# Optimization experiments

Measured on AMD Instinct MI355X. Metric: run time of the kernel, lower is better.

## Reference

```python
import jax, jax.numpy as jnp
import numpy as np

B, L, D, H, HD, K, MLP = 4, 2048, 1024, 16, 64, 24, 4096


def setup_inputs() -> dict:
    key = jax.random.key(0)
    ks = jax.random.split(key, 17)
    f32 = jnp.float32
    rn = lambda k, s, sc=1.0: jax.random.normal(k, s, dtype=f32) * sc
    return {
        'inputs': rn(ks[0], (B, L, D)),
        'eig_vals': jax.random.uniform(ks[1], (K,), dtype=f32),  # positive eigenvalues
        'eig_vecs': rn(ks[2], (L, K), 1.0 / np.sqrt(L)),
        'w_filters': rn(ks[3], (K, D), 1.0 / np.sqrt(K)),        # lecun_normal-ish
        'w_inputs': rn(ks[4], (D, D), 1.0 / np.sqrt(D)),
        'ln1_scale': jnp.ones((D,), f32),
        'ln1_bias': jnp.zeros((D,), f32),
        'wq': rn(ks[5], (D, H, HD), 1.0 / np.sqrt(D)),
        'wk': rn(ks[6], (D, H, HD), 1.0 / np.sqrt(D)),
        'wv': rn(ks[7], (D, H, HD), 1.0 / np.sqrt(D)),
        'wo': rn(ks[8], (H, HD, D), 1.0 / np.sqrt(D)),
        'ln2_scale': jnp.ones((D,), f32),
        'ln2_bias': jnp.zeros((D,), f32),
        'mlp_w1': rn(ks[9], (D, MLP), 1.0 / np.sqrt(D)),
        'mlp_b1': jnp.zeros((MLP,), f32),
        'mlp_w2': rn(ks[10], (MLP, D), 1.0 / np.sqrt(MLP)),
        'mlp_b2': jnp.zeros((D,), f32),
    }


def _layer_norm(x, scale, bias, eps=1e-6):
    m = jnp.mean(x, axis=-1, keepdims=True)
    v = jnp.var(x, axis=-1, keepdims=True)
    return (x - m) * jax.lax.rsqrt(v + eps) * scale + bias


def reference(inputs, eig_vals, eig_vecs, w_filters, w_inputs,
              ln1_scale, ln1_bias, wq, wk, wv, wo,
              ln2_scale, ln2_bias, mlp_w1, mlp_b1, mlp_w2, mlp_b2):
    seq = inputs.shape[1]
    # --- STU spectral long convolution ---
    rescaled = eig_vecs * eig_vals[None, :] ** 0.25            # [L,K]
    filters = jnp.einsum('lk,kd->ld', rescaled, w_filters)      # [L,D]
    xi = jnp.einsum('bli,id->bld', inputs, w_inputs)            # [B,L,D]
    # causal per-channel conv: out[b,l,d] = sum_t filters[t,d]*xi[b,l-t,d]
    # == full convolve truncated to first L; do it as one batched FFT conv.
    n = 2 * seq
    F = jnp.fft.rfft(filters, n=n, axis=0)                      # [n//2+1, D]
    X = jnp.fft.rfft(xi, n=n, axis=1)                           # [B, n//2+1, D]
    projection = jnp.fft.irfft(X * F[None], n=n, axis=1)[:, :seq, :]
    stu_outs = projection                                       # make_stu_residual=False

    # --- self attention (pre-LN) ---
    x = _layer_norm(stu_outs, ln1_scale, ln1_bias)
    hd = wq.shape[-1]
    q = jnp.einsum('bld,dhk->blhk', x, wq) / jnp.sqrt(jnp.asarray(hd, x.dtype))
    k = jnp.einsum('bld,dhk->blhk', x, wk)
    v = jnp.einsum('bld,dhk->blhk', x, wv)
    attn = jax.nn.softmax(jnp.einsum('bqhk,bshk->bhqs', q, k), axis=-1)
    a = jnp.einsum('bhqs,bshk->bqhk', attn, v)
    a = jnp.einsum('bqhk,hkd->bqd', a, wo)
    x = a + stu_outs

    # --- MLP block (pre-LN) ---
    y = _layer_norm(x, ln2_scale, ln2_bias)
    y = jax.nn.gelu(jnp.einsum('bld,df->blf', y, mlp_w1) + mlp_b1)
    y = jnp.einsum('blf,fd->bld', y, mlp_w2) + mlp_b2
    return x + y
```

## Files before the change

kernel.cpp:

```cpp
#include <hip/hip_runtime.h>
#include <math.h>

#define B_ 4
#define L_ 2048
#define D_ 1024
#define H_ 16
#define HD_ 64
#define K_ 24
#define MLP_ 4096

typedef unsigned short u16;
typedef short s16x8 __attribute__((ext_vector_type(8)));
typedef float fx4 __attribute__((ext_vector_type(4)));
typedef _Float16 h2 __attribute__((ext_vector_type(2)));

__device__ __forceinline__ u16 f2bf(float f) {
    unsigned u = __float_as_uint(f);
    unsigned r = (u + 0x7fff + ((u >> 16) & 1)) >> 16;
    return (u16)r;
}

__device__ __forceinline__ u16 f2h(float f) {
    _Float16 hv = (_Float16)f;
    return __builtin_bit_cast(u16, hv);
}

__device__ __forceinline__ float gelu_t(float x) {
    float u = 0.7978845608028654f * (x + 0.044715f * x * x * x);
    return x / (1.f + __expf(-2.f * u));
}

__device__ __forceinline__ void gload_lds16(const void* g, void* l) {
    __builtin_amdgcn_global_load_lds(
        (const __attribute__((address_space(1))) unsigned int*)g,
        (__attribute__((address_space(3))) unsigned int*)l, 16, 0, 0);
}

#define SBAR() do { __builtin_amdgcn_sched_barrier(0); \
                    __builtin_amdgcn_s_barrier(); \
                    __builtin_amdgcn_sched_barrier(0); } while (0)

__global__ __launch_bounds__(256) void filters_T(const float* __restrict__ eig_vals,
                                                 const float* __restrict__ eig_vecs,
                                                 const float* __restrict__ w_filters,
                                                 u16* __restrict__ outT) {
    int l0 = blockIdx.x * 64, d0 = blockIdx.y * 64;
    __shared__ float ev25[K_];
    __shared__ float rr[64][25];
    __shared__ float wfs[K_][64];
    int tid = threadIdx.x;
    if (tid < K_) ev25[tid] = powf(eig_vals[tid], 0.25f);
    __syncthreads();
    for (int i = tid; i < 64 * K_; i += 256)
        rr[i / K_][i % K_] = eig_vecs[l0 * K_ + i];
    for (int i = tid; i < K_ * 64; i += 256) {
        int k = i >> 6, dd = i & 63;
        wfs[k][dd] = ev25[k] * w_filters[k * D_ + d0 + dd];
    }
    __syncthreads();
    int lane = tid & 63, w = tid >> 6;
    float acc[16];
#pragma unroll
    for (int i = 0; i < 16; i++) acc[i] = 0.f;
#pragma unroll
    for (int k = 0; k < K_; k++) {
        float rv = rr[lane][k];
#pragma unroll
        for (int i = 0; i < 16; i++) acc[i] += rv * wfs[k][w * 16 + i];
    }
#pragma unroll
    for (int i = 0; i < 16; i++)
        outT[(size_t)(d0 + w * 16 + i) * L_ + l0 + (lane ^ 63)] = f2h(acc[i]);
}

__global__ __launch_bounds__(256) void transpose_h(const u16* __restrict__ in,
                                                   u16* __restrict__ outT) {
    __shared__ u16 t[64][68];
    int m0 = blockIdx.x * 64, d0 = blockIdx.y * 64;
    int tid = threadIdx.x;
    int r = tid >> 3, c8 = (tid & 7) * 8;
#pragma unroll
    for (int p = 0; p < 2; p++) {
        uint4 X = *(const uint4*)&in[(size_t)(m0 + r + p * 32) * D_ + d0 + c8];
        *(uint2*)&t[r + p * 32][c8] = make_uint2(X.x, X.y);
        *(uint2*)&t[r + p * 32][c8 + 4] = make_uint2(X.z, X.w);
    }
    __syncthreads();
    int dr = tid >> 3, mc = (tid & 7) * 8;
#pragma unroll
    for (int p = 0; p < 2; p++) {
        int d = dr + p * 32;
        unsigned h[8];
#pragma unroll
        for (int j = 0; j < 8; j++) h[j] = t[mc + j][d];
        uint4 o;
        o.x = h[0] | (h[1] << 16); o.y = h[2] | (h[3] << 16);
        o.z = h[4] | (h[5] << 16); o.w = h[6] | (h[7] << 16);
        *(uint4*)&outT[(size_t)(d0 + d) * (size_t)(B_ * L_) + m0 + mc] = o;
    }
}

__global__ __launch_bounds__(256) void cast_bf16(const float* __restrict__ in,
                                                 u16* __restrict__ out) {
    int i = blockIdx.x * 256 + threadIdx.x;
    float4 v = ((const float4*)in)[i];
    ushort4 o;
    o.x = f2bf(v.x); o.y = f2bf(v.y); o.z = f2bf(v.z); o.w = f2bf(v.w);
    ((ushort4*)out)[i] = o;
}

struct CastJobs {
    const float* src[8];
    u16* dst[8];
    int R[8], C[8];
    int off[8];
};

__global__ __launch_bounds__(256) void cast_T_all(CastJobs J) {
    __shared__ float t[32][33];
    int bid = blockIdx.x;
    int j = 0;
#pragma unroll
    for (int k = 1; k < 8; k++)
        if (bid >= J.off[k]) j = k;
    int local = bid - J.off[j];
    int R = J.R[j], C = J.C[j];
    int nbx = C >> 5;
    int lsh = __ffs(nbx) - 1;
    int bx = local & (nbx - 1), by = local >> lsh;
    const float* in = J.src[j];
    u16* out = J.dst[j];
    int c0 = bx * 32, r0 = by * 32;
    int tx = threadIdx.x & 31, ty = threadIdx.x >> 5;
#pragma unroll
    for (int p = 0; p < 4; p++)
        t[ty + p * 8][tx] = in[(size_t)(r0 + ty + p * 8) * C + c0 + tx];
    __syncthreads();
#pragma unroll
    for (int p = 0; p < 4; p++)
        out[(size_t)(c0 + ty + p * 8) * R + r0 + tx] = f2bf(t[tx][ty + p * 8]);
}

__global__ __launch_bounds__(512, 2) void gemm_bf16(
    const u16* __restrict__ A, const u16* __restrict__ Bt,
    float* __restrict__ C, u16* __restrict__ Cb,
    int M, int N, int K, float alpha,
    const float* __restrict__ bias, const float* __restrict__ resid, int act,
    int qcols, int f16out) {
    __shared__ __align__(16) u16 lds[3 * 24576];
    const int SLOT = 24576;
    const int BOFF = 8192;

    int tid = threadIdx.x;
    int wid = tid >> 6, lane = tid & 63;
    int quad = lane >> 4, l15 = lane & 15;
    int rb = wid >> 2, cb = wid & 3;

    int bxs = blockIdx.x, bys = blockIdx.y;
    if ((gridDim.y & 7) == 0) {
        int bid = blockIdx.x + gridDim.x * blockIdx.y;
        int xcd = bid & 7, idx = bid >> 3;
        bys = xcd + 8 * (idx / gridDim.x);
        bxs = idx % gridDim.x;
    }
    int bm = bys * 128, bn = bxs * 256;
    int nt = K >> 6;

    int qoffe = (quad * 8) ^ ((l15 & 4) ? 16 : 0);
    int aRd = (rb * 64 + l15) * 64 + qoffe;
    int bRd = BOFF + (cb * 64 + l15) * 64 + qoffe;

    int srow = wid * 8 + (lane >> 3);
    int scole = ((lane & 7) * 8) ^ ((lane & 32) ? 16 : 0);
    const u16* Ag = A + (size_t)(bm + srow) * K + scole;
    const u16* Bg = Bt + (size_t)(bn + srow) * K + scole;
    int ldst = wid * 512;

#define STAGE_A(s, t, c) gload_lds16(Ag + (size_t)(c) * 64 * K + (size_t)(t) * 64, \
                                     &lds[(s) * SLOT + (c) * 4096 + ldst])
#define STAGE_B(s, t, c) gload_lds16(Bg + (size_t)(c) * 64 * K + (size_t)(t) * 64, \
                                     &lds[(s) * SLOT + BOFF + (c) * 4096 + ldst])

    STAGE_A(0, 0, 0); STAGE_A(0, 0, 1);
    STAGE_B(0, 0, 0); STAGE_B(0, 0, 1); STAGE_B(0, 0, 2); STAGE_B(0, 0, 3);
    STAGE_A(1, 1, 0); STAGE_A(1, 1, 1);
    STAGE_B(1, 1, 0); STAGE_B(1, 1, 1); STAGE_B(1, 1, 2); STAGE_B(1, 1, 3);
    asm volatile("s_waitcnt vmcnt(6)" ::: "memory");
    SBAR();

    fx4 acc[4][4];
#pragma unroll
    for (int i = 0; i < 4; i++)
#pragma unroll
        for (int j = 0; j < 4; j++) acc[i][j] = (fx4){0.f, 0.f, 0.f, 0.f};

    int sa = 0, sb = 1, sc = 2;
    for (int t = 0; t < nt; t++) {
        int ts = (t + 2 < nt) ? t + 2 : nt - 1;
        const u16* ap = &lds[sa * SLOT + aRd];
        const u16* bp = &lds[sa * SLOT + bRd];
        s16x8 a[4], b[2][4];
#pragma unroll
        for (int mf = 0; mf < 4; mf++) a[mf] = *(const s16x8*)(ap + mf * 1024);
#pragma unroll
        for (int kk = 0; kk < 2; kk++)
#pragma unroll
            for (int nf = 0; nf < 4; nf++)
                b[kk][nf] = *(const s16x8*)(bp + nf * 1024 + kk * 32);
        STAGE_A(sc, ts, 0); STAGE_A(sc, ts, 1); STAGE_B(sc, ts, 0);
        SBAR();
        asm volatile("s_waitcnt lgkmcnt(0)" ::: "memory");
        __builtin_amdgcn_sched_barrier(0);
        __builtin_amdgcn_s_setprio(1);
#pragma unroll
        for (int nf = 0; nf < 4; nf++)
#pragma unroll
            for (int mf = 0; mf < 4; mf++)
                acc[mf][nf] = __builtin_amdgcn_mfma_f32_16x16x32_bf16(
                    a[mf], b[0][nf], acc[mf][nf], 0, 0, 0);
        __builtin_amdgcn_s_setprio(0);
        SBAR();
#pragma unroll
        for (int mf = 0; mf < 4; mf++)
            a[mf] = *(const s16x8*)(ap + mf * 1024 + 32);
        STAGE_B(sc, ts, 1); STAGE_B(sc, ts, 2); STAGE_B(sc, ts, 3);
        SBAR();
        asm volatile("s_waitcnt lgkmcnt(0)" ::: "memory");
        __builtin_amdgcn_sched_barrier(0);
        __builtin_amdgcn_s_setprio(1);
#pragma unroll
        for (int nf = 0; nf < 4; nf++)
#pragma unroll
            for (int mf = 0; mf < 4; mf++)
                acc[mf][nf] = __builtin_amdgcn_mfma_f32_16x16x32_bf16(
                    a[mf], b[1][nf], acc[mf][nf], 0, 0, 0);
        __builtin_amdgcn_s_setprio(0);
        asm volatile("s_waitcnt vmcnt(6)" ::: "memory");
        __builtin_amdgcn_sched_barrier(0);
        SBAR();
        int tmp = sa; sa = sb; sb = sc; sc = tmp;
    }
#undef STAGE_A
#undef STAGE_B

#pragma unroll
    for (int mf = 0; mf < 4; mf++) {
        int row0 = bm + rb * 64 + mf * 16 + quad * 4;
#pragma unroll
        for (int nf = 0; nf < 4; nf++) {
            int col = bn + cb * 64 + nf * 16 + l15;
            float a2 = (col < qcols) ? alpha * 0.125f : alpha;
            float bv = bias ? bias[col] : 0.f;
#pragma unroll
            for (int reg = 0; reg < 4; reg++) {
                float v = a2 * acc[mf][nf][reg] + bv;
                if (act) v = gelu_t(v);
                size_t idx = (size_t)(row0 + reg) * N + col;
                if (resid) v += resid[idx];
                if (C) C[idx] = v;
                else Cb[idx] = f16out ? f2h(v) : f2bf(v);
            }
        }
    }
}

__global__ __launch_bounds__(256, 6) void conv_k(const u16* __restrict__ FT,
                                                 const u16* __restrict__ XT,
                                                 float* __restrict__ OUT) {
    int bid = blockIdx.x + 16 * (blockIdx.y + 16 * blockIdx.z);
    int xcd = bid & 7, ix = bid >> 3;
    int group = xcd * 8 + (ix >> 4);
    int xblk = ix & 15;
    int d0 = (group & 15) * 64, b = group >> 4;

    __shared__ u16 xs[64][132];
    __shared__ u16 ftr[64][68];
    int tid = threadIdx.x;
    int dd = tid & 63;
    int jg = tid >> 6;
    int L0 = jg * 16;
    int frow = tid >> 3, fq = (tid & 7) * 8;
    int xrow = tid >> 4, xq = (tid & 15) * 8;
    const u16* fbase = FT + (size_t)(d0 + frow) * L_ + fq;
    const u16* xbase = XT + (size_t)(d0 + xrow) * (B_ * L_) + (size_t)b * L_ + xq;

#pragma unroll 1
    for (int half = 0; half < 2; half++) {
        int lt = half ? (31 - xblk) : xblk;
        int l0 = lt * 64;
        float acc[16];
#pragma unroll
        for (int i = 0; i < 16; i++) acc[i] = 0.f;

        for (int t0 = 0; t0 <= l0; t0 += 64) {
            int jb = l0 - t0 - 64;
#pragma unroll
            for (int p = 0; p < 2; p++) {
                uint4 Fq = *(const uint4*)(fbase + (size_t)p * 32 * L_ + t0);
                *(uint2*)&ftr[frow + p * 32][fq] = make_uint2(Fq.x, Fq.y);
                *(uint2*)&ftr[frow + p * 32][fq + 4] = make_uint2(Fq.z, Fq.w);
            }
            if (jb >= 0) {
#pragma unroll
                for (int p = 0; p < 4; p++) {
                    uint4 Xq = *(const uint4*)(xbase + (size_t)p * 16 * (B_ * L_) + jb);
                    *(uint2*)&xs[xrow + p * 16][xq] = make_uint2(Xq.x, Xq.y);
                    *(uint2*)&xs[xrow + p * 16][xq + 4] = make_uint2(Xq.z, Xq.w);
                }
            } else {
#pragma unroll
                for (int p = 0; p < 4; p++) {
                    uint4 Xq = make_uint4(0, 0, 0, 0);
                    if (xq >= 64)
                        Xq = *(const uint4*)(xbase + (size_t)p * 16 * (B_ * L_) - 64);
                    *(uint2*)&xs[xrow + p * 16][xq] = make_uint2(Xq.x, Xq.y);
                    *(uint2*)&xs[xrow + p * 16][xq + 4] = make_uint2(Xq.z, Xq.w);
                }
            }
            __syncthreads();

            unsigned Q[10], E[10];
            {
                uint2 q0 = *(const uint2*)&xs[dd][L0];
                uint2 q1 = *(const uint2*)&xs[dd][L0 + 4];
                uint2 q2 = *(const uint2*)&xs[dd][L0 + 8];
                uint2 q3 = *(const uint2*)&xs[dd][L0 + 12];
                Q[0] = q0.x; Q[1] = q0.y; Q[2] = q1.x; Q[3] = q1.y;
                Q[4] = q2.x; Q[5] = q2.y; Q[6] = q3.x; Q[7] = q3.y;
#pragma unroll
                for (int j = 0; j < 7; j++)
                    E[j] = __builtin_amdgcn_alignbit(Q[j + 1], Q[j], 16);
            }
#pragma unroll
            for (int s = 0; s < 16; s++) {
                const int h = (2 * s) % 10;
                uint2 nx = *(const uint2*)&xs[dd][L0 + 16 + 4 * s];
                Q[(h + 8) % 10] = nx.x;
                Q[(h + 9) % 10] = nx.y;
                E[(h + 7) % 10] = __builtin_amdgcn_alignbit(Q[(h + 8) % 10], Q[(h + 7) % 10], 16);
                E[(h + 8) % 10] = __builtin_amdgcn_alignbit(Q[(h + 9) % 10], Q[(h + 8) % 10], 16);
                uint2 fr = *(const uint2*)&ftr[dd][4 * s];
                h2 f01 = __builtin_bit_cast(h2, fr.x);
                h2 f23 = __builtin_bit_cast(h2, fr.y);
#pragma unroll
                for (int i = 0; i < 16; i += 2) {
                    const int p = (h + i / 2) % 10;
                    const int p1 = (h + i / 2 + 1) % 10;
                    const int p2 = (h + i / 2 + 2) % 10;
                    acc[i] = __builtin_amdgcn_fdot2(f01, __builtin_bit_cast(h2, E[p]), acc[i], false);
                    acc[i] = __builtin_amdgcn_fdot2(f23, __builtin_bit_cast(h2, E[p1]), acc[i], false);
                    acc[i + 1] = __builtin_amdgcn_fdot2(f01, __builtin_bit_cast(h2, Q[p1]), acc[i + 1], false);
                    acc[i + 1] = __builtin_amdgcn_fdot2(f23, __builtin_bit_cast(h2, Q[p2]), acc[i + 1], false);
                }
            }
            __syncthreads();
        }
#pragma unroll
        for (int i = 0; i < 16; i++)
            OUT[((size_t)b * L_ + l0 + L0 + i) * D_ + d0 + dd] = acc[i];
    }
}

__global__ __launch_bounds__(256) void layernorm_bf16(const float* __restrict__ x,
                                                      const float* __restrict__ scale,
                                                      const float* __restrict__ bias,
                                                      u16* __restrict__ y) {
    size_t row = blockIdx.x;
    int tid = threadIdx.x;
    const float4 v = *(const float4*)&x[row * D_ + tid * 4];
    float s = v.x + v.y + v.z + v.w;
    float q = v.x * v.x + v.y * v.y + v.z * v.z + v.w * v.w;
#pragma unroll
    for (int off = 32; off >= 1; off >>= 1) {
        s += __shfl_xor(s, off, 64);
        q += __shfl_xor(q, off, 64);
    }
    __shared__ float ss[4], sq[4];
    int w = tid >> 6;
    if ((tid & 63) == 0) { ss[w] = s; sq[w] = q; }
    __syncthreads();
    s = ss[0] + ss[1] + ss[2] + ss[3];
    q = sq[0] + sq[1] + sq[2] + sq[3];
    float mean = s * (1.f / D_);
    float var = q * (1.f / D_) - mean * mean;
    float r = rsqrtf(var + 1e-6f);
    const float4 sc = *(const float4*)&scale[tid * 4];
    const float4 bi = *(const float4*)&bias[tid * 4];
    ushort4 o;
    o.x = f2bf((v.x - mean) * r * sc.x + bi.x);
    o.y = f2bf((v.y - mean) * r * sc.y + bi.y);
    o.z = f2bf((v.z - mean) * r * sc.z + bi.z);
    o.w = f2bf((v.w - mean) * r * sc.w + bi.w);
    *(ushort4*)&y[row * D_ + tid * 4] = o;
}

__global__ __launch_bounds__(256) void attn_mfma(const u16* __restrict__ Qg,
                                                 const u16* __restrict__ Kg,
                                                 const u16* __restrict__ Vg,
                                                 u16* __restrict__ Og) {
    const int QSTR = 3072;
    int bxs = blockIdx.x, bys = blockIdx.y;
    {
        int bid = blockIdx.x + gridDim.x * blockIdx.y;
        int xcd = bid & 7, idx = bid >> 3;
        bys = xcd + 8 * (idx / gridDim.x);
        bxs = idx % gridDim.x;
    }
    int q0 = bxs * 128;
    int b = bys >> 4, h = bys & 15;
    __shared__ __align__(16) u16 qs[128 * 72];
    __shared__ __align__(16) u16 ks[64 * 72];
    __shared__ __align__(16) u16 vt[64 * 72];
    int tid = threadIdx.x;
    int w = tid >> 6, lane = tid & 63;
    int quad = lane >> 4, l15 = lane & 15;
    const size_t base = (size_t)b * L_ * QSTR + h * HD_;

#pragma unroll
    for (int i = tid; i < 128 * 8; i += 256) {
        int r = i >> 3, c = i & 7;
        *(uint4*)&qs[r * 72 + c * 8] =
            *(const uint4*)&Qg[base + (size_t)(q0 + r) * QSTR + c * 8];
    }
    __syncthreads();
    s16x8 aq[2][2];
#pragma unroll
    for (int mi = 0; mi < 2; mi++)
#pragma unroll
        for (int kb = 0; kb < 2; kb++)
            aq[mi][kb] = *(const s16x8*)&qs[(w * 32 + mi * 16 + l15) * 72 + kb * 32 + quad * 8];

    float rsacc[2][4];
    fx4 o[2][4];
#pragma unroll
    for (int mi = 0; mi < 2; mi++)
#pragma unroll
        for (int i = 0; i < 4; i++) {
            rsacc[mi][i] = 0.f;
            o[mi][i] = (fx4){0.f, 0.f, 0.f, 0.f};
        }
    u16* psw = qs + w * 32 * 72;

    int kr0 = tid >> 3, kc = tid & 7;
    const u16* kg0 = Kg + base + (size_t)kr0 * QSTR + kc * 8;
    const u16* kg1 = kg0 + (size_t)32 * QSTR;
    const u16* vg = Vg + base + (size_t)lane * QSTR + w * 8;
    uint4 kp0 = *(const uint4*)kg0;
    uint4 kp1 = *(const uint4*)kg1;
    uint4 vp0 = *(const uint4*)vg;
    uint4 vp1 = *(const uint4*)(vg + 32);

    for (int s0 = 0; s0 < L_; s0 += 64) {
        __syncthreads();
        *(uint4*)&ks[kr0 * 72 + kc * 8] = kp0;
        *(uint4*)&ks[(kr0 + 32) * 72 + kc * 8] = kp1;
        {
            u16 t0[8], t1[8];
            *(uint4*)t0 = vp0;
            *(uint4*)t1 = vp1;
#pragma unroll
            for (int j = 0; j < 8; j++) vt[(w * 8 + j) * 72 + lane] = t0[j];
#pragma unroll
            for (int j = 0; j < 8; j++) vt[(w * 8 + 32 + j) * 72 + lane] = t1[j];
        }
        if (s0 + 64 < L_) {
            size_t off = (size_t)(s0 + 64) * QSTR;
            kp0 = *(const uint4*)(kg0 + off);
            kp1 = *(const uint4*)(kg1 + off);
            vp0 = *(const uint4*)(vg + off);
            vp1 = *(const uint4*)(vg + off + 32);
        }
        __syncthreads();

        fx4 sv[2][4];
#pragma unroll
        for (int mi = 0; mi < 2; mi++)
#pragma unroll
            for (int nt = 0; nt < 4; nt++) sv[mi][nt] = (fx4){0.f, 0.f, 0.f, 0.f};
#pragma unroll
        for (int kb = 0; kb < 2; kb++)
#pragma unroll
            for (int nt = 0; nt < 4; nt++) {
                s16x8 bk = *(const s16x8*)&ks[(nt * 16 + l15) * 72 + kb * 32 + quad * 8];
#pragma unroll
                for (int mi = 0; mi < 2; mi++)
                    sv[mi][nt] = __builtin_amdgcn_mfma_f32_16x16x32_bf16(
                        aq[mi][kb], bk, sv[mi][nt], 0, 0, 0);
            }

#pragma unroll
        for (int mi = 0; mi < 2; mi++)
#pragma unroll
            for (int nt = 0; nt < 4; nt++)
#pragma unroll
                for (int reg = 0; reg < 4; reg++) {
                    float p = __expf(sv[mi][nt][reg]);
                    rsacc[mi][reg] += p;
                    psw[(mi * 16 + quad * 4 + reg) * 72 + nt * 16 + l15] = f2bf(p);
                }

#pragma unroll
        for (int kb = 0; kb < 2; kb++) {
            s16x8 ap[2];
#pragma unroll
            for (int mi = 0; mi < 2; mi++)
                ap[mi] = *(const s16x8*)&psw[(mi * 16 + l15) * 72 + kb * 32 + quad * 8];
#pragma unroll
            for (int nt = 0; nt < 4; nt++) {
                s16x8 bv = *(const s16x8*)&vt[(nt * 16 + l15) * 72 + kb * 32 + quad * 8];
#pragma unroll
                for (int mi = 0; mi < 2; mi++)
                    o[mi][nt] = __builtin_amdgcn_mfma_f32_16x16x32_bf16(
                        ap[mi], bv, o[mi][nt], 0, 0, 0);
            }
        }
    }
    float lsum[2][4];
#pragma unroll
    for (int mi = 0; mi < 2; mi++)
#pragma unroll
        for (int reg = 0; reg < 4; reg++) {
            float r = rsacc[mi][reg];
#pragma unroll
            for (int off = 8; off >= 1; off >>= 1)
                r += __shfl_xor(r, off, 16);
            lsum[mi][reg] = r;
        }
    const size_t baseo = (size_t)b * L_ * 1024 + h * HD_;
#pragma unroll
    for (int mi = 0; mi < 2; mi++)
#pragma unroll
        for (int reg = 0; reg < 4; reg++) {
            float inv = 1.f / lsum[mi][reg];
            size_t row = baseo +
                (size_t)(q0 + w * 32 + mi * 16 + quad * 4 + reg) * 1024;
#pragma unroll
            for (int nt = 0; nt < 4; nt++)
                Og[row + nt * 16 + l15] = f2bf(o[mi][nt][reg] * inv);
        }
}

extern "C" void kernel_launch(void* const* d_in, const int* in_sizes, int n_in,
                              void* d_out, int out_size, void* d_ws, size_t ws_size,
                              hipStream_t stream) {
    const float* inputs   = (const float*)d_in[0];
    const float* eig_vals = (const float*)d_in[1];
    const float* eig_vecs = (const float*)d_in[2];
    const float* w_filt   = (const float*)d_in[3];
    const float* w_inp    = (const float*)d_in[4];
    const float* ln1_s    = (const float*)d_in[5];
    const float* ln1_b    = (const float*)d_in[6];
    const float* wq       = (const float*)d_in[7];
    const float* wk       = (const float*)d_in[8];
    const float* wv       = (const float*)d_in[9];
    const float* wo       = (const float*)d_in[10];
    const float* ln2_s    = (const float*)d_in[11];
    const float* ln2_b    = (const float*)d_in[12];
    const float* w1       = (const float*)d_in[13];
    const float* b1       = (const float*)d_in[14];
    const float* w2       = (const float*)d_in[15];
    const float* b2       = (const float*)d_in[16];
    float* out = (float*)d_out;
    char* ws = (char*)d_ws;
    const size_t MB = 1u << 20;
    u16*   INb   = (u16*)(ws + 0 * MB);
    u16*   WIt   = (u16*)(ws + 16 * MB);
    u16*   WQKVt = (u16*)(ws + 18 * MB);
    u16*   WOt   = (u16*)(ws + 24 * MB);
    u16*   W1t   = (u16*)(ws + 26 * MB);
    u16*   W2t   = (u16*)(ws + 34 * MB);
    u16*   XIH   = (u16*)(ws + 48 * MB);
    u16*   HID   = (u16*)(ws + 48 * MB);
    u16*   XIT   = (u16*)(ws + 64 * MB);
    float* STU   = (float*)(ws + 80 * MB);
    u16*   XN    = (u16*)(ws + 112 * MB);
    u16*   QKV   = (u16*)(ws + 128 * MB);
    float* Xb    = (float*)(ws + 128 * MB);
    u16*   YN    = (u16*)(ws + 160 * MB);
    u16*   FvT   = (u16*)(ws + 176 * MB);
    u16*   Ab    = (u16*)(ws + 176 * MB);

    const int M = B_ * L_;

    cast_bf16<<<(M * D_ / 4 + 255) / 256, 256, 0, stream>>>(inputs, INb);

    CastJobs J;
    J.src[0] = w_inp; J.dst[0] = WIt;               J.R[0] = D_;   J.C[0] = D_;
    J.src[1] = wq;    J.dst[1] = WQKVt + 0 * D_ * D_; J.R[1] = D_; J.C[1] = D_;
    J.src[2] = wk;    J.dst[2] = WQKVt + 1 * D_ * D_; J.R[2] = D_; J.C[2] = D_;
    J.src[3] = wv;    J.dst[3] = WQKVt + 2 * D_ * D_; J.R[3] = D_; J.C[3] = D_;
    J.src[4] = wo;    J.dst[4] = WOt;               J.R[4] = D_;   J.C[4] = D_;
    J.src[5] = w1;    J.dst[5] = W1t;               J.R[5] = D_;   J.C[5] = MLP_;
    J.src[6] = w2;    J.dst[6] = W2t;               J.R[6] = MLP_; J.C[6] = D_;
    J.src[7] = w_inp; J.dst[7] = WIt;               J.R[7] = D_;   J.C[7] = D_;
    int nb = 0;
    for (int j = 0; j < 7; j++) {
        J.off[j] = nb;
        nb += (J.C[j] / 32) * (J.R[j] / 32);
    }
    J.off[7] = nb;
    cast_T_all<<<nb, 256, 0, stream>>>(J);

    filters_T<<<dim3(L_ / 64, D_ / 64), 256, 0, stream>>>(eig_vals, eig_vecs, w_filt, FvT);

    gemm_bf16<<<dim3(D_ / 256, M / 128), 512, 0, stream>>>(
        INb, WIt, nullptr, XIH, M, D_, D_, 1.f, nullptr, nullptr, 0, 0, 1);
    transpose_h<<<dim3(M / 64, D_ / 64), 256, 0, stream>>>(XIH, XIT);
    conv_k<<<dim3(16, D_ / 64, B_), 256, 0, stream>>>(FvT, XIT, STU);
    layernorm_bf16<<<M, 256, 0, stream>>>(STU, ln1_s, ln1_b, XN);
    gemm_bf16<<<dim3(3 * D_ / 256, M / 128), 512, 0, stream>>>(
        XN, WQKVt, nullptr, QKV, M, 3 * D_, D_, 1.f, nullptr, nullptr, 0, D_, 0);
    attn_mfma<<<dim3(L_ / 128, B_ * H_), 256, 0, stream>>>(
        QKV, QKV + D_, QKV + 2 * D_, Ab);
    gemm_bf16<<<dim3(D_ / 256, M / 128), 512, 0, stream>>>(
        Ab, WOt, Xb, nullptr, M, D_, D_, 1.f, nullptr, STU, 0, 0, 0);
    layernorm_bf16<<<M, 256, 0, stream>>>(Xb, ln2_s, ln2_b, YN);
    gemm_bf16<<<dim3(MLP_ / 256, M / 128), 512, 0, stream>>>(
        YN, W1t, nullptr, HID, M, MLP_, D_, 1.f, b1, nullptr, 1, 0, 0);
    gemm_bf16<<<dim3(D_ / 256, M / 128), 512, 0, stream>>>(
        HID, W2t, out, nullptr, M, D_, MLP_, 1.f, b2, Xb, 0, 0, 0);
}
```

Before: 821.1 us.

## Fuse transpose into GEMM epilogue and tune attention softmax packing and priority

The xi GEMM now writes its f16 output already transposed by staging the tile in LDS and storing columns contiguously. This removes the separate transpose_h kernel and its extra read and write of an 8192x1024 f16 tensor. The attention kernel also raises wave priority around its MFMA blocks and packs pairs of bf16 probabilities with v_cvt_pk_bf16_f32. The epilogue adds an LDS round trip and syncs, and the packed conversion rounds differently from the manual f2bf.

```diff
diff --git a/kernel.cpp b/kernel.cpp
--- a/kernel.cpp
+++ b/kernel.cpp
@@ -73,33 +73,6 @@
         outT[(size_t)(d0 + w * 16 + i) * L_ + l0 + (lane ^ 63)] = f2h(acc[i]);
 }
 
-__global__ __launch_bounds__(256) void transpose_h(const u16* __restrict__ in,
-                                                   u16* __restrict__ outT) {
-    __shared__ u16 t[64][68];
-    int m0 = blockIdx.x * 64, d0 = blockIdx.y * 64;
-    int tid = threadIdx.x;
-    int r = tid >> 3, c8 = (tid & 7) * 8;
-#pragma unroll
-    for (int p = 0; p < 2; p++) {
-        uint4 X = *(const uint4*)&in[(size_t)(m0 + r + p * 32) * D_ + d0 + c8];
-        *(uint2*)&t[r + p * 32][c8] = make_uint2(X.x, X.y);
-        *(uint2*)&t[r + p * 32][c8 + 4] = make_uint2(X.z, X.w);
-    }
-    __syncthreads();
-    int dr = tid >> 3, mc = (tid & 7) * 8;
-#pragma unroll
-    for (int p = 0; p < 2; p++) {
-        int d = dr + p * 32;
-        unsigned h[8];
-#pragma unroll
-        for (int j = 0; j < 8; j++) h[j] = t[mc + j][d];
-        uint4 o;
-        o.x = h[0] | (h[1] << 16); o.y = h[2] | (h[3] << 16);
-        o.z = h[4] | (h[5] << 16); o.w = h[6] | (h[7] << 16);
-        *(uint4*)&outT[(size_t)(d0 + d) * (size_t)(B_ * L_) + m0 + mc] = o;
-    }
-}
-
 __global__ __launch_bounds__(256) void cast_bf16(const float* __restrict__ in,
                                                  u16* __restrict__ out) {
     int i = blockIdx.x * 256 + threadIdx.x;
@@ -243,6 +216,31 @@
 #undef STAGE_A
 #undef STAGE_B
 
+    if (f16out) {
+        asm volatile("s_waitcnt vmcnt(0)" ::: "memory");
+        __syncthreads();
+        u16* tb = lds;
+#pragma unroll
+        for (int mf = 0; mf < 4; mf++)
+#pragma unroll
+            for (int nf = 0; nf < 4; nf++) {
+                int c = cb * 64 + nf * 16 + l15;
+                int r = rb * 64 + mf * 16 + quad * 4;
+#pragma unroll
+                for (int reg = 0; reg < 4; reg++)
+                    tb[c * 136 + r + reg] = f2h(acc[mf][nf][reg]);
+            }
+        __syncthreads();
+#pragma unroll
+        for (int it = 0; it < 8; it++) {
+            int c = (tid >> 4) + it * 32;
+            int r0 = (tid & 15) * 8;
+            uint4 v4 = *(const uint4*)&tb[c * 136 + r0];
+            *(uint4*)&Cb[(size_t)(bn + c) * M + bm + r0] = v4;
+        }
+        return;
+    }
+
 #pragma unroll
     for (int mf = 0; mf < 4; mf++) {
         int row0 = bm + rb * 64 + mf * 16 + quad * 4;
@@ -258,7 +256,7 @@
                 size_t idx = (size_t)(row0 + reg) * N + col;
                 if (resid) v += resid[idx];
                 if (C) C[idx] = v;
-                else Cb[idx] = f16out ? f2h(v) : f2bf(v);
+                else Cb[idx] = f2bf(v);
             }
         }
     }
@@ -477,6 +475,7 @@
         for (int mi = 0; mi < 2; mi++)
 #pragma unroll
             for (int nt = 0; nt < 4; nt++) sv[mi][nt] = (fx4){0.f, 0.f, 0.f, 0.f};
+        __builtin_amdgcn_s_setprio(1);
 #pragma unroll
         for (int kb = 0; kb < 2; kb++)
 #pragma unroll
@@ -487,18 +486,29 @@
                     sv[mi][nt] = __builtin_amdgcn_mfma_f32_16x16x32_bf16(
                         aq[mi][kb], bk, sv[mi][nt], 0, 0, 0);
             }
+        __builtin_amdgcn_s_setprio(0);
 
 #pragma unroll
         for (int mi = 0; mi < 2; mi++)
 #pragma unroll
-            for (int nt = 0; nt < 4; nt++)
-#pragma unroll
-                for (int reg = 0; reg < 4; reg++) {
-                    float p = __expf(sv[mi][nt][reg]);
-                    rsacc[mi][reg] += p;
-                    psw[(mi * 16 + quad * 4 + reg) * 72 + nt * 16 + l15] = f2bf(p);
-                }
-
+            for (int nt = 0; nt < 4; nt++) {
+                float p0 = __expf(sv[mi][nt][0]);
+                float p1 = __expf(sv[mi][nt][1]);
+                float p2 = __expf(sv[mi][nt][2]);
+                float p3 = __expf(sv[mi][nt][3]);
+                rsacc[mi][0] += p0; rsacc[mi][1] += p1;
+                rsacc[mi][2] += p2; rsacc[mi][3] += p3;
+                unsigned pk01, pk23;
+                asm("v_cvt_pk_bf16_f32 %0, %1, %2" : "=v"(pk01) : "v"(p0), "v"(p1));
+                asm("v_cvt_pk_bf16_f32 %0, %1, %2" : "=v"(pk23) : "v"(p2), "v"(p3));
+                int basei = (mi * 16 + quad * 4) * 72 + nt * 16 + l15;
+                psw[basei]       = (u16)pk01;
+                psw[basei + 72]  = (u16)(pk01 >> 16);
+                psw[basei + 144] = (u16)pk23;
+                psw[basei + 216] = (u16)(pk23 >> 16);
+            }
+
+        __builtin_amdgcn_s_setprio(1);
 #pragma unroll
         for (int kb = 0; kb < 2; kb++) {
             s16x8 ap[2];
@@ -514,6 +524,7 @@
                         ap[mi], bv, o[mi][nt], 0, 0, 0);
             }
         }
+        __builtin_amdgcn_s_setprio(0);
     }
     float lsum[2][4];
 #pragma unroll
@@ -569,7 +580,6 @@
     u16*   WOt   = (u16*)(ws + 24 * MB);
     u16*   W1t   = (u16*)(ws + 26 * MB);
     u16*   W2t   = (u16*)(ws + 34 * MB);
-    u16*   XIH   = (u16*)(ws + 48 * MB);
     u16*   HID   = (u16*)(ws + 48 * MB);
     u16*   XIT   = (u16*)(ws + 64 * MB);
     float* STU   = (float*)(ws + 80 * MB);
@@ -604,8 +614,7 @@
     filters_T<<<dim3(L_ / 64, D_ / 64), 256, 0, stream>>>(eig_vals, eig_vecs, w_filt, FvT);
 
     gemm_bf16<<<dim3(D_ / 256, M / 128), 512, 0, stream>>>(
-        INb, WIt, nullptr, XIH, M, D_, D_, 1.f, nullptr, nullptr, 0, 0, 1);
-    transpose_h<<<dim3(M / 64, D_ / 64), 256, 0, stream>>>(XIH, XIT);
+        INb, WIt, nullptr, XIT, M, D_, D_, 1.f, nullptr, nullptr, 0, 0, 1);
     conv_k<<<dim3(16, D_ / 64, B_), 256, 0, stream>>>(FvT, XIT, STU);
     layernorm_bf16<<<M, 256, 0, stream>>>(STU, ln1_s, ln1_b, XN);
     gemm_bf16<<<dim3(3 * D_ / 256, M / 128), 512, 0, stream>>>(
```

Measured after the change: 806.1 us. Within noise of the previous version (-1.8%).
